# Kernel tuning notes

Hardware: AMD Instinct MI355X
Metric: run time of the kernel (lower is better)

## Reference

```python
import jax, jax.numpy as jnp
import numpy as np

N, D = 8192, 256

def _gram_rbf(x, y, sigma):
    x2 = jnp.sum(x * x, axis=-1)                      # [N]
    y2 = jnp.sum(y * y, axis=-1)                      # [M]
    xy = jnp.einsum('nd,md->nm', x, y)                # [N,M] GEMM
    sq = x2[:, None] + y2[None, :] - 2.0 * xy
    return jnp.exp(-sq / sigma)

def setup_inputs() -> dict:
    key = jax.random.key(0)
    k1, k2 = jax.random.split(key)
    return {
        'input': jax.random.normal(k1, (N, D), dtype=jnp.float32),
        'target': jax.random.normal(k2, (N, D), dtype=jnp.float32) + 0.5,
        'sigma': 256,
    }

def reference(input, target, sigma):
    XX = _gram_rbf(input, input, sigma)
    YY = _gram_rbf(target, target, sigma)
    XY = _gram_rbf(input, target, sigma)
    return jnp.mean(XX) + jnp.mean(YY) - 2.0 * jnp.mean(XY)
```

## Files before the change

### kernel.cpp

```cpp
#include <hip/hip_runtime.h>
#include <hip/hip_bf16.h>
#include <stdint.h>
#include <stddef.h>


#define N_PTS   8192
#define DIM     256
#define TWO_N   16384

#define AS1 __attribute__((address_space(1)))
#define AS3 __attribute__((address_space(3)))

typedef __attribute__((ext_vector_type(4))) float f32x4;
typedef __attribute__((ext_vector_type(4))) int   i32x4;
typedef __attribute__((ext_vector_type(8))) int   i32x8;

__global__ __launch_bounds__(256) void mmd_prep(const float* __restrict__ X,
                                                const float* __restrict__ Y,
                                                const int* __restrict__ sigmap,
                                                unsigned char* __restrict__ Zf8,
                                                float* __restrict__ n2,
                                                float* __restrict__ part) {
    if (blockIdx.x == 0 && threadIdx.x < 64) part[threadIdx.x] = 0.0f;

    const int wave = threadIdx.x >> 6;
    const int lane = threadIdx.x & 63;
    const int row  = blockIdx.x * 4 + wave;

    const float* src = (row < N_PTS) ? (X + (size_t)row * DIM)
                                     : (Y + (size_t)(row - N_PTS) * DIM);
    float4 v = ((const float4*)src)[lane];

    float s = v.x * v.x + v.y * v.y + v.z * v.z + v.w * v.w;
#pragma unroll
    for (int off = 32; off; off >>= 1) s += __shfl_down(s, off, 64);
    if (lane == 0) {
        const float c2 = -1.4426950408889634f / (float)(*sigmap);
        n2[row] = c2 * s;
    }

    const int p01 = __builtin_amdgcn_cvt_pk_fp8_f32(v.x, v.y, 0, false);
    const int p23 = __builtin_amdgcn_cvt_pk_fp8_f32(v.z, v.w, 0, false);
    const unsigned int pk = ((unsigned)p01 & 0xffffu) | ((unsigned)p23 << 16);
    *(unsigned int*)(Zf8 + (size_t)row * DIM + (size_t)lane * 4) = pk;
}

__global__ __launch_bounds__(256, 4) void mmd_main(const unsigned char* __restrict__ Zf8,
                                                   const float* __restrict__ n2,
                                                   const int* __restrict__ sigmap,
                                                   float* __restrict__ part) {
    __shared__ char smem_b[32768];
    __shared__ float wsum[4];

    const int bid = (int)blockIdx.x;
    const int p   = bid >> 4;
    const int cc  = bid & 15;
    const int r0  = p;
    const int r1  = 127 - p;

    const int nT0 = (cc <= r0) ? (((r0 - cc) >> 4) + 1) : 0;
    const int nT1 = ((r1 - cc) >> 4) + 1;
    const int nS0 = nT0 * 2;
    const int nS  = nS0 + nT1 * 2;

    const int t    = threadIdx.x;
    const int wave = t >> 6;
    const int lane = t & 63;
    const int g    = lane >> 4;
    const int ml   = lane & 15;

    const float m2 = 2.8853900817779268f / (float)(*sigmap);
    const int   SC = 0x7f7f7f7f;

    const int gbase = (t >> 4) * 256 + (((t & 15) ^ (t >> 4)) * 16);
    const int lbase = t * 16;

    int rb0[2], rb1[2];
#pragma unroll
    for (int kc = 0; kc < 2; ++kc) {
        rb0[kc] = ml * 256 + (((kc * 8 + g * 2)     ^ ml) * 16);
        rb1[kc] = ml * 256 + (((kc * 8 + g * 2 + 1) ^ ml) * 16);
    }

    i32x8 af[2][2];
    float a_i[2][4];
    auto loadA = [&](int rowTile) {
        const int rowBase = rowTile * 128;
#pragma unroll
        for (int mt = 0; mt < 2; ++mt) {
            const unsigned char* rp =
                Zf8 + (size_t)(rowBase + wave * 32 + mt * 16 + ml) * 256 + g * 32;
#pragma unroll
            for (int kc = 0; kc < 2; ++kc) {
                union { i32x4 h[2]; i32x8 v; } u;
                u.h[0] = *(const i32x4*)(rp + kc * 128);
                u.h[1] = *(const i32x4*)(rp + kc * 128 + 16);
                af[mt][kc] = u.v;
            }
        }
#pragma unroll
        for (int mt = 0; mt < 2; ++mt)
#pragma unroll
            for (int rr = 0; rr < 4; ++rr)
                a_i[mt][rr] = n2[rowBase + wave * 32 + mt * 16 + g * 4 + rr];
    };

    const int firstRow = nT0 ? r0 : r1;
    loadA(firstRow);
    int curRow = firstRow;

    const f32x4 zacc = {0.0f, 0.0f, 0.0f, 0.0f};

    auto sliceCol = [&](int s, int& rowT, int& bc, int& h) {
        int si;
        if (s < nS0) { rowT = r0; si = s; }
        else         { rowT = r1; si = s - nS0; }
        bc = cc + (si >> 2) * 16 * 2;
        bc = cc + ((si >> 1) * 16);
        h  = si & 1;
    };

    {
        int rT, bc, h; sliceCol(0, rT, bc, h);
        const unsigned char* sb = Zf8 + (size_t)(bc * 128 + h * 64) * 256 + gbase;
#pragma unroll
        for (int i = 0; i < 4; ++i)
            __builtin_amdgcn_global_load_lds((const AS1 void*)(sb + i * 4096),
                                             (AS3 void*)(smem_b + i * 4096 + lbase), 16, 0, 0);
    }

    float block_acc = 0.0f;
    int cur = 0;

    for (int s = 0; s < nS; ++s) {
        int rowT, bc, h;
        sliceCol(s, rowT, bc, h);
        if (rowT != curRow) { loadA(rowT); curRow = rowT; }
        const int colBase = bc * 128 + h * 64;

        float eb[4];
#pragma unroll
        for (int nt = 0; nt < 4; ++nt)
            eb[nt] = __builtin_amdgcn_exp2f(n2[colBase + nt * 16 + ml]);

        __syncthreads();

        if (s + 1 < nS) {
            int rTN, bcN, hN;
            sliceCol(s + 1, rTN, bcN, hN);
            const unsigned char* sb =
                Zf8 + (size_t)(bcN * 128 + hN * 64) * 256 + gbase;
            char* dst = smem_b + (cur ^ 1) * 16384;
#pragma unroll
            for (int i = 0; i < 4; ++i)
                __builtin_amdgcn_global_load_lds((const AS1 void*)(sb + i * 4096),
                                                 (AS3 void*)(dst + i * 4096 + lbase), 16, 0, 0);
        }

        const char* buf = smem_b + cur * 16384;
        f32x4 acc[2][4];
#pragma unroll
        for (int nt = 0; nt < 4; ++nt) {
#pragma unroll
            for (int kc = 0; kc < 2; ++kc) {
                union { i32x4 hh[2]; i32x8 v; } u;
                u.hh[0] = *(const i32x4*)(buf + nt * 4096 + rb0[kc]);
                u.hh[1] = *(const i32x4*)(buf + nt * 4096 + rb1[kc]);
                const i32x8 bf = u.v;
#pragma unroll
                for (int mt = 0; mt < 2; ++mt)
                    acc[mt][nt] = __builtin_amdgcn_mfma_scale_f32_16x16x128_f8f6f4(
                        af[mt][kc], bf, (kc == 0) ? zacc : acc[mt][nt],
                        0, 0, 0, SC, 0, SC);
            }
        }

        float ts0 = 0.0f, ts1 = 0.0f, ts2 = 0.0f, ts3 = 0.0f;
#pragma unroll
        for (int mt = 0; mt < 2; ++mt)
#pragma unroll
            for (int nt = 0; nt < 4; ++nt) {
                const float e = eb[nt];
                ts0 = fmaf(__builtin_amdgcn_exp2f(fmaf(acc[mt][nt][0], m2, a_i[mt][0])), e, ts0);
                ts1 = fmaf(__builtin_amdgcn_exp2f(fmaf(acc[mt][nt][1], m2, a_i[mt][1])), e, ts1);
                ts2 = fmaf(__builtin_amdgcn_exp2f(fmaf(acc[mt][nt][2], m2, a_i[mt][2])), e, ts2);
                ts3 = fmaf(__builtin_amdgcn_exp2f(fmaf(acc[mt][nt][3], m2, a_i[mt][3])), e, ts3);
            }
        const float tsum = (ts0 + ts1) + (ts2 + ts3);

        const float sgn = ((bc < 64) == (rowT < 64)) ? 1.0f : -1.0f;
        const float w   = (bc == rowT) ? sgn : 2.0f * sgn;
        block_acc = fmaf(w, tsum, block_acc);
        cur ^= 1;
    }

    float s = block_acc;
#pragma unroll
    for (int off = 32; off; off >>= 1) s += __shfl_down(s, off, 64);
    if (lane == 0) wsum[wave] = s;
    __syncthreads();
    if (t == 0)
        atomicAdd(part + (bid & 63), wsum[0] + wsum[1] + wsum[2] + wsum[3]);
}

__global__ __launch_bounds__(64) void mmd_finish(const float* __restrict__ part,
                                                 float* __restrict__ out) {
    const int lane = threadIdx.x & 63;
    float s = part[lane];
#pragma unroll
    for (int off = 32; off; off >>= 1) s += __shfl_down(s, off, 64);
    if (lane == 0) out[0] = s * (1.0f / 67108864.0f);
}

extern "C" void kernel_launch(void* const* d_in, const int* in_sizes, int n_in,
                              void* d_out, int out_size, void* d_ws, size_t ws_size,
                              hipStream_t stream) {
    const float* X      = (const float*)d_in[0];
    const float* Y      = (const float*)d_in[1];
    const int*   sigmap = (const int*)d_in[2];
    float*       out    = (float*)d_out;

    unsigned char* Zf8  = (unsigned char*)d_ws;
    float*         n2   = (float*)((char*)d_ws + (size_t)TWO_N * DIM);
    float*         part = n2 + TWO_N;

    mmd_prep<<<TWO_N / 4, 256, 0, stream>>>(X, Y, sigmap, Zf8, n2, part);
    mmd_main<<<64 * 16, 256, 0, stream>>>(Zf8, n2, sigmap, part);
    mmd_finish<<<1, 64, 0, stream>>>(part, out);
}
```

Before: 114.1 us.

## Deepen LDS prefetch to two slices ahead with explicit waitcnt and barriers

```diff
diff --git a/kernel.cpp b/kernel.cpp
--- a/kernel.cpp
+++ b/kernel.cpp
@@ -14,6 +14,12 @@
 typedef __attribute__((ext_vector_type(4))) float f32x4;
 typedef __attribute__((ext_vector_type(4))) int   i32x4;
 typedef __attribute__((ext_vector_type(8))) int   i32x8;
+
+#define WAIT_VM4()  asm volatile("s_waitcnt vmcnt(4)" ::: "memory")
+#define WAIT_VM0()  asm volatile("s_waitcnt vmcnt(0)" ::: "memory")
+#define WAIT_LGKM() asm volatile("s_waitcnt lgkmcnt(0)" ::: "memory")
+#define SCHEDB()    __builtin_amdgcn_sched_barrier(0)
+#define BARRIER()   __builtin_amdgcn_s_barrier()
 
 __global__ __launch_bounds__(256) void mmd_prep(const float* __restrict__ X,
                                                 const float* __restrict__ Y,
@@ -105,29 +111,33 @@
                 a_i[mt][rr] = n2[rowBase + wave * 32 + mt * 16 + g * 4 + rr];
     };
 
-    const int firstRow = nT0 ? r0 : r1;
-    loadA(firstRow);
-    int curRow = firstRow;
-
-    const f32x4 zacc = {0.0f, 0.0f, 0.0f, 0.0f};
-
     auto sliceCol = [&](int s, int& rowT, int& bc, int& h) {
         int si;
         if (s < nS0) { rowT = r0; si = s; }
         else         { rowT = r1; si = s - nS0; }
-        bc = cc + (si >> 2) * 16 * 2;
         bc = cc + ((si >> 1) * 16);
         h  = si & 1;
     };
 
-    {
-        int rT, bc, h; sliceCol(0, rT, bc, h);
+    auto stageTo = [&](char* dstBuf, int s) {
+        int rT, bc, h; sliceCol(s, rT, bc, h);
         const unsigned char* sb = Zf8 + (size_t)(bc * 128 + h * 64) * 256 + gbase;
 #pragma unroll
         for (int i = 0; i < 4; ++i)
             __builtin_amdgcn_global_load_lds((const AS1 void*)(sb + i * 4096),
-                                             (AS3 void*)(smem_b + i * 4096 + lbase), 16, 0, 0);
-    }
+                                             (AS3 void*)(dstBuf + i * 4096 + lbase), 16, 0, 0);
+    };
+
+    const int firstRow = nT0 ? r0 : r1;
+    loadA(firstRow);
+    int curRow = firstRow;
+
+    const f32x4 zacc = {0.0f, 0.0f, 0.0f, 0.0f};
+
+    stageTo(smem_b,         0);
+    stageTo(smem_b + 16384, 1);
+    WAIT_VM4();
+    SCHEDB(); BARRIER(); SCHEDB();
 
     float block_acc = 0.0f;
     int cur = 0;
@@ -138,27 +148,14 @@
         if (rowT != curRow) { loadA(rowT); curRow = rowT; }
         const int colBase = bc * 128 + h * 64;
 
-        float eb[4];
+        float ebl[4];
 #pragma unroll
         for (int nt = 0; nt < 4; ++nt)
-            eb[nt] = __builtin_amdgcn_exp2f(n2[colBase + nt * 16 + ml]);
-
-        __syncthreads();
-
-        if (s + 1 < nS) {
-            int rTN, bcN, hN;
-            sliceCol(s + 1, rTN, bcN, hN);
-            const unsigned char* sb =
-                Zf8 + (size_t)(bcN * 128 + hN * 64) * 256 + gbase;
-            char* dst = smem_b + (cur ^ 1) * 16384;
-#pragma unroll
-            for (int i = 0; i < 4; ++i)
-                __builtin_amdgcn_global_load_lds((const AS1 void*)(sb + i * 4096),
-                                                 (AS3 void*)(dst + i * 4096 + lbase), 16, 0, 0);
-        }
+            ebl[nt] = n2[colBase + nt * 16 + ml];
 
         const char* buf = smem_b + cur * 16384;
         f32x4 acc[2][4];
+        __builtin_amdgcn_s_setprio(1);
 #pragma unroll
         for (int nt = 0; nt < 4; ++nt) {
 #pragma unroll
@@ -174,8 +171,19 @@
                         0, 0, 0, SC, 0, SC);
             }
         }
+        __builtin_amdgcn_s_setprio(0);
+
+        WAIT_LGKM();
+        SCHEDB(); BARRIER(); SCHEDB();
+
+        const bool more = (s + 2 < nS);
+        if (more) stageTo(smem_b + cur * 16384, s + 2);
 
         float ts0 = 0.0f, ts1 = 0.0f, ts2 = 0.0f, ts3 = 0.0f;
+        float eb[4];
+#pragma unroll
+        for (int nt = 0; nt < 4; ++nt)
+            eb[nt] = __builtin_amdgcn_exp2f(ebl[nt]);
 #pragma unroll
         for (int mt = 0; mt < 2; ++mt)
 #pragma unroll
@@ -191,6 +199,9 @@
         const float sgn = ((bc < 64) == (rowT < 64)) ? 1.0f : -1.0f;
         const float w   = (bc == rowT) ? sgn : 2.0f * sgn;
         block_acc = fmaf(w, tsum, block_acc);
+
+        if (more) { WAIT_VM4(); } else { WAIT_VM0(); }
+        SCHEDB(); BARRIER(); SCHEDB();
         cur ^= 1;
     }
 
```

After: 114.1 us. About the same (+0.1%).
